# Kernel optimization log

Hardware: AMD Instinct MI355X
Metric: run time of the kernel (lower is better)

The kernel has to match this reference:

```python
import jax, jax.numpy as jnp
import numpy as np

B, K, N, D, H, DD, NB, SEQ = 1, 512, 16384, 512, 64, 64, 10, 2048
COREF_PROP = 1  # config['coref_prop']
BIG = 1e23      # additive mask penalty from the torch code


def bucket_distance(d):
    # Lee et al. style log buckets: 0,1,2,3,4, [5-7], [8-15], [16-31], [32-63], [64+]
    d = jnp.abs(d)
    logb = jnp.floor(jnp.log2(jnp.maximum(d, 1).astype(jnp.float32))).astype(d.dtype) + 3
    return jnp.clip(jnp.where(d < 5, d, logb), 0, NB - 1)


def setup_inputs() -> dict:
    key = jax.random.key(0)
    ks = jax.random.split(key, 20)
    rng = np.random.default_rng(0)
    s = 0.02
    span_begin = jnp.sort(jax.random.randint(ks[2], (B, K), 0, SEQ), axis=-1)
    return dict(
        all_span_vecs=jax.random.normal(ks[0], (B, N, D), jnp.float32),
        span_vecs=jax.random.normal(ks[1], (B, K, D), jnp.float32),
        span_begin=span_begin,
        span_end=span_begin + jax.random.randint(ks[3], (B, K), 1, 10),
        triangular_mask=jnp.broadcast_to(jnp.tril(jnp.ones((K, K), jnp.float32), -1), (B, K, K)),
        span_scores=jax.random.normal(ks[4], (B, K, 1), jnp.float32),
        prune_indices=jnp.asarray(np.sort(np.stack([rng.choice(N, K, replace=False) for _ in range(B)]), axis=-1), jnp.int32),
        span_lengths=jnp.full((B,), K, jnp.int32),
        sequence_lengths=jnp.full((B,), SEQ, jnp.int32),
        Wl=jax.random.normal(ks[5], (D, H)) * s, bl=jnp.zeros((H,), jnp.float32),
        Wr=jax.random.normal(ks[6], (D, H)) * s, br=jnp.zeros((H,), jnp.float32),
        Wp=jax.random.normal(ks[7], (D, H)) * s,
        dist_emb=jax.random.normal(ks[8], (NB, DD)) * s,
        Wd=jax.random.normal(ks[9], (DD, H)) * s, bd=jnp.zeros((H,), jnp.float32),
        Wo=jax.random.normal(ks[10], (H, 1)) * s, bo=jnp.zeros((1,), jnp.float32),
        Wg1=jax.random.normal(ks[11], (2 * D, D)) * s, bg1=jnp.zeros((D,), jnp.float32),
        Wg2=jax.random.normal(ks[12], (2 * D, D)) * s, bg2=jnp.zeros((D,), jnp.float32),
        Wpr=jax.random.normal(ks[13], (D, 1)) * s, bpr=jnp.zeros((1,), jnp.float32),
    )


def reference(all_span_vecs, span_vecs, span_begin, span_end, triangular_mask,
              span_scores, prune_indices, span_lengths, sequence_lengths,
              Wl, bl, Wr, br, Wp, dist_emb, Wd, bd, Wo, bo,
              Wg1, bg1, Wg2, bg2, Wpr, bpr):
    # ----- OptFFpairs pairwise scorer: relu(left_i + right_j + prod(v_i*v_j) + dist_ij) -> scalar
    dist_idx = bucket_distance(span_begin[:, :, None] - span_begin[:, None, :])  # [B,K,K]
    dist_feat = dist_emb[dist_idx] @ Wd + bd                                     # [B,K,K,H]

    def pair_scores(u):
        left = u @ Wl + bl                                  # [B,K,H]
        right = u @ Wr + br                                 # [B,K,H]
        prod = jnp.einsum('bid,bjd,dh->bijh', u, u, Wp)     # avoids [B,K,K,D] intermediate
        h = jax.nn.relu(left[:, :, None, :] + right[:, None, :, :] + prod + dist_feat)
        return (h @ Wo + bo)[..., 0]                        # [B,K,K], i.e. squeeze(-1)

    eye = jnp.eye(K, dtype=span_vecs.dtype)[None]

    def add_scores(cs, ss):  # coref_add_scores: add span scores as rows+cols, zero diagonal
        cs = cs + ss + jnp.swapaxes(ss, -1, -2)
        return cs * (1.0 - eye)

    def gate(Wg, bg, left, right):  # MyGate: g = sigmoid(W[l;r]); g*l + (1-g)*r
        g = jax.nn.sigmoid(jnp.concatenate([left, right], -1) @ Wg + bg)
        return g * left + (1.0 - g) * right

    update = span_vecs
    cs = add_scores(pair_scores(update), span_scores)
    m1 = (1.0 - triangular_mask) * BIG
    m2 = (1.0 - jnp.swapaxes(triangular_mask, 1, 2)) * BIG
    for _ in range(COREF_PROP):
        p1 = jax.nn.softmax(cs - m1, axis=-1)
        p2 = jax.nn.softmax(cs - m2, axis=-1)
        c1 = p1 @ update
        c2 = p2 @ update
        update = gate(Wg1, bg1, update, c1) + gate(Wg2, bg2, update, c2)
        # update_coref_scores=True: rescore with pruner(update)
        cs = add_scores(pair_scores(update), update @ Wpr + bpr)

    # ----- overwrite_spans: masked scatter of updated filtered spans into all spans
    mask = (jnp.arange(K)[None, :] < span_lengths[:, None])[..., None]  # [B,K,1]
    b_idx = jnp.arange(B)[:, None]
    orig = all_span_vecs[b_idx, prune_indices]                          # [B,K,D]
    all_out = all_span_vecs.at[b_idx, prune_indices].set(jnp.where(mask, update, orig))
    return all_out, update, cs
```

## Files before the change

kernel.cpp:

```cpp
#include <hip/hip_runtime.h>
#include <hip/hip_bf16.h>


typedef __bf16 bf16;
typedef bf16 bf16x8 __attribute__((ext_vector_type(8)));
typedef float f32x4 __attribute__((ext_vector_type(4)));
typedef float f32x16 __attribute__((ext_vector_type(16)));

#define MFMA16(a, b, c) __builtin_amdgcn_mfma_f32_16x16x32_bf16((a), (b), (c), 0, 0, 0)
#define MFMA32(a, b, c) __builtin_amdgcn_mfma_f32_32x32x16_bf16((a), (b), (c), 0, 0, 0)

__device__ __forceinline__ void gll16(const bf16* g, bf16* lds) {
  __builtin_amdgcn_global_load_lds(
      (const __attribute__((address_space(1))) unsigned int*)g,
      (__attribute__((address_space(3))) unsigned int*)lds, 16, 0, 0);
}

__global__ void k_prep(const float* __restrict__ sv,
                       const float* __restrict__ Wl, const float* __restrict__ Wr,
                       const float* __restrict__ Wg1, const float* __restrict__ Wg2,
                       const float* __restrict__ de, const float* __restrict__ Wd,
                       const float* __restrict__ bd, const float* __restrict__ bl,
                       const float* __restrict__ br, const float* __restrict__ bg1,
                       const float* __restrict__ bg2, const float* __restrict__ Wp,
                       bf16* __restrict__ u1, bf16* __restrict__ ugb,
                       bf16* __restrict__ wlr, float* __restrict__ blbr,
                       float* __restrict__ bgc, bf16* __restrict__ wgb,
                       float* __restrict__ dtab, bf16* __restrict__ wpTb)
{
  const int total = 262144 + 65536 + 128 + 1048576 + 1024 + 640 + 32768;
  for (int idx0 = blockIdx.x * 256 + threadIdx.x; idx0 < total; idx0 += 2048 * 256) {
    int k = idx0;
    if (k < 262144) {
      float v = sv[k]; bf16 b = (bf16)v; u1[k] = b;
      int i = k >> 9, d = k & 511;
      ugb[(long)i * 1024 + d] = b;
      ugb[524288 + (long)i * 1024 + d] = b;
      continue;
    }
    k -= 262144;
    if (k < 65536) {
      int d = k >> 7, h = k & 127;
      wlr[k] = (bf16)(h < 64 ? Wl[d * 64 + h] : Wr[d * 64 + h - 64]);
      continue;
    }
    k -= 65536;
    if (k < 128) { blbr[k] = (k < 64 ? bl[k] : br[k - 64]); continue; }
    k -= 128;
    if (k < 1048576) {
      wgb[k] = (bf16)(k < 524288 ? Wg1[k] : Wg2[k - 524288]);
      continue;
    }
    k -= 1048576;
    if (k < 1024) { bgc[k] = (k < 512 ? bg1[k] : bg2[k - 512]); continue; }
    k -= 1024;
    if (k < 640) {
      int b_ = k >> 6, h = k & 63;
      float s = bd[h];
      for (int e = 0; e < 64; ++e) s += de[b_ * 64 + e] * Wd[e * 64 + h];
      dtab[k] = s;
      continue;
    }
    k -= 640;
    {
      int h = k >> 9, d = k & 511;
      wpTb[k] = (bf16)Wp[d * 64 + h];
    }
  }
}

__global__ __launch_bounds__(256, 2) void k_gemm(
    const bf16* __restrict__ A, int lda, long asz,
    const bf16* __restrict__ B, int ldb, long bsz,
    float* __restrict__ C, int ldc, long csz,
    const float* __restrict__ bias, int bstride, int K,
    bf16* __restrict__ xout)
{
  __shared__ bf16 As[64 * 40];
  __shared__ bf16 Bs[64 * 40];
  const int t = threadIdx.x, lane = t & 63, wave = t >> 6;
  const int tc = blockIdx.x, tr = blockIdx.y, z = blockIdx.z;
  A += (long)z * asz; B += (long)z * bsz; C += (long)z * csz;
  const int wr = wave >> 1, wc = wave & 1;
  const int arow = t >> 2, aslot = t & 3;
  const int s = lane >> 4, rr = lane & 15;
  f32x4 acc00 = {}, acc01 = {}, acc10 = {}, acc11 = {};
  const int nk = K >> 5;
  for (int kk = 0; kk < nk; ++kk) {
    __syncthreads();
    *(uint4*)&As[arow * 40 + aslot * 8] =
        *(const uint4*)(A + (long)(tr * 64 + arow) * lda + kk * 32 + aslot * 8);
    {
      const bf16* bsrc = B + (long)(kk * 32 + aslot * 8) * ldb + tc * 64 + arow;
      bf16x8 tv;
#pragma unroll
      for (int e = 0; e < 8; ++e) tv[e] = bsrc[(long)e * ldb];
      *(bf16x8*)&Bs[arow * 40 + aslot * 8] = tv;
    }
    __syncthreads();
    bf16x8 a0 = *(const bf16x8*)&As[(wr * 32 + rr) * 40 + s * 8];
    bf16x8 a1 = *(const bf16x8*)&As[(wr * 32 + 16 + rr) * 40 + s * 8];
    bf16x8 b0 = *(const bf16x8*)&Bs[(wc * 32 + rr) * 40 + s * 8];
    bf16x8 b1 = *(const bf16x8*)&Bs[(wc * 32 + 16 + rr) * 40 + s * 8];
    acc00 = MFMA16(a0, b0, acc00);
    acc01 = MFMA16(a0, b1, acc01);
    acc10 = MFMA16(a1, b0, acc10);
    acc11 = MFMA16(a1, b1, acc11);
  }
#pragma unroll
  for (int mf = 0; mf < 2; ++mf) {
#pragma unroll
    for (int nf = 0; nf < 2; ++nf) {
      f32x4 v = mf == 0 ? (nf == 0 ? acc00 : acc01) : (nf == 0 ? acc10 : acc11);
      int col = tc * 64 + wc * 32 + nf * 16 + rr;
      float bi = bias ? bias[z * bstride + col] : 0.f;
      int row0 = tr * 64 + wr * 32 + mf * 16 + s * 4;
#pragma unroll
      for (int r = 0; r < 4; ++r) {
        float val = v[r] + bi;
        int row = row0 + r;
        C[(long)row * ldc + col] = val;
        if (xout) {
          long gidx = (row < 512)
              ? ((long)row * 1024 + 512 + col)
              : (524288 + (long)(row - 512) * 1024 + 512 + col);
          xout[gidx] = (bf16)val;
        }
      }
    }
  }
}

__global__ __launch_bounds__(512, 2) void k_pair(
    const bf16* __restrict__ Ubf, const float* __restrict__ Uf,
    const bf16* __restrict__ wpTb, const float* __restrict__ LR,
    const float* __restrict__ dtabg, const int* __restrict__ sb,
    const float* __restrict__ ss, const float* __restrict__ Wo,
    const float* __restrict__ bo, float* __restrict__ cs,
    const float* __restrict__ copysrc, float* __restrict__ copydst, int docopy)
{
  __shared__ bf16 As[2][512 * 32];
  __shared__ bf16 Vs[2][64 * 32];
  __shared__ float uil[512];
  __shared__ float dts[640];

  const int t = threadIdx.x;
  const int l = t & 63;
  const int w = t >> 6;
  const int i = blockIdx.x;
  const int half = l >> 5;
  const int l31 = l & 31;

  if (t < 128) {
    float4 v = *(const float4*)(Uf + (long)i * 512 + t * 4);
    *(float4*)&uil[t * 4] = v;
  }
  for (int idx = t; idx < 640; idx += 512) dts[idx] = dtabg[idx];

  const bf16 *asrc0, *asrc1, *asrc2, *asrc3;
  {
    int rq0 = 0 * 128 + (t >> 2), rq1 = 1 * 128 + (t >> 2);
    int rq2 = 2 * 128 + (t >> 2), rq3 = 3 * 128 + (t >> 2);
    asrc0 = Ubf + (long)rq0 * 512 + (((t & 3) ^ ((rq0 >> 1) & 3)) * 8);
    asrc1 = Ubf + (long)rq1 * 512 + (((t & 3) ^ ((rq1 >> 1) & 3)) * 8);
    asrc2 = Ubf + (long)rq2 * 512 + (((t & 3) ^ ((rq2 >> 1) & 3)) * 8);
    asrc3 = Ubf + (long)rq3 * 512 + (((t & 3) ^ ((rq3 >> 1) & 3)) * 8);
  }
  int aoff[2][2], voff[2][2];
#pragma unroll
  for (int jf = 0; jf < 2; ++jf)
#pragma unroll
    for (int ks = 0; ks < 2; ++ks) {
      int r = w * 64 + jf * 32 + l31;
      aoff[jf][ks] = r * 64 + (((ks * 2 + half) ^ ((r >> 1) & 3)) * 16);
    }
#pragma unroll
  for (int hf = 0; hf < 2; ++hf)
#pragma unroll
    for (int ks = 0; ks < 2; ++ks) {
      int h = hf * 32 + l31;
      voff[hf][ks] = h * 64 + (((ks * 2 + half) ^ ((h >> 1) & 3)) * 16);
    }
  const int vh = t >> 2;
  const int vcp = (t & 3) ^ ((vh >> 1) & 3);

  __syncthreads();

  gll16(asrc0, &As[0][0 * 4096 + w * 512]);
  gll16(asrc1, &As[0][1 * 4096 + w * 512]);
  gll16(asrc2, &As[0][2 * 4096 + w * 512]);
  gll16(asrc3, &As[0][3 * 4096 + w * 512]);
  if (t < 256) {
    bf16x8 wv = *(const bf16x8*)(wpTb + (long)vh * 512 + vcp * 8);
    float4 u0 = *(const float4*)&uil[vcp * 8];
    float4 u1 = *(const float4*)&uil[vcp * 8 + 4];
    bf16x8 sv8;
#pragma unroll
    for (int e = 0; e < 4; ++e) {
      sv8[e] = (bf16)((float)wv[e] * u0[e]);
      sv8[e + 4] = (bf16)((float)wv[e + 4] * u1[e]);
    }
    *(bf16x8*)((char*)&Vs[0][0] + vh * 64 + (t & 3) * 16) = sv8;
  }
  asm volatile("s_waitcnt vmcnt(0)");
  __syncthreads();

  f32x16 acc[2][2] = {};

  for (int kc = 0; kc < 16; ++kc) {
    const int cur = kc & 1;
    if (kc < 15) {
      gll16(asrc0 + (kc + 1) * 32, &As[cur ^ 1][0 * 4096 + w * 512]);
      gll16(asrc1 + (kc + 1) * 32, &As[cur ^ 1][1 * 4096 + w * 512]);
      gll16(asrc2 + (kc + 1) * 32, &As[cur ^ 1][2 * 4096 + w * 512]);
      gll16(asrc3 + (kc + 1) * 32, &As[cur ^ 1][3 * 4096 + w * 512]);
      if (t < 256) {
        bf16x8 wv = *(const bf16x8*)(wpTb + (long)vh * 512 + (kc + 1) * 32 + vcp * 8);
        float4 u0 = *(const float4*)&uil[(kc + 1) * 32 + vcp * 8];
        float4 u1 = *(const float4*)&uil[(kc + 1) * 32 + vcp * 8 + 4];
        bf16x8 sv8;
#pragma unroll
        for (int e = 0; e < 4; ++e) {
          sv8[e] = (bf16)((float)wv[e] * u0[e]);
          sv8[e + 4] = (bf16)((float)wv[e + 4] * u1[e]);
        }
        *(bf16x8*)((char*)&Vs[cur ^ 1][0] + vh * 64 + (t & 3) * 16) = sv8;
      }
    }
    const char* Asb = (const char*)&As[cur][0];
    const char* Vsb = (const char*)&Vs[cur][0];
#pragma unroll
    for (int ks = 0; ks < 2; ++ks) {
      bf16x8 af0 = *(const bf16x8*)(Asb + aoff[0][ks]);
      bf16x8 af1 = *(const bf16x8*)(Asb + aoff[1][ks]);
      bf16x8 vf0 = *(const bf16x8*)(Vsb + voff[0][ks]);
      bf16x8 vf1 = *(const bf16x8*)(Vsb + voff[1][ks]);
      __builtin_amdgcn_s_setprio(1);
      acc[0][0] = MFMA32(af0, vf0, acc[0][0]);
      acc[0][1] = MFMA32(af0, vf1, acc[0][1]);
      acc[1][0] = MFMA32(af1, vf0, acc[1][0]);
      acc[1][1] = MFMA32(af1, vf1, acc[1][1]);
      __builtin_amdgcn_s_setprio(0);
    }
    if (kc < 15) asm volatile("s_waitcnt vmcnt(0)");
    __syncthreads();
  }

  const float lf0 = LR[i * 128 + l31];
  const float lf1 = LR[i * 128 + 32 + l31];
  const float wo0 = Wo[l31], wo1 = Wo[32 + l31];
  const int sbi = sb[i];
  const float ssi = ss[i];
  const float bo0 = bo[0];
#pragma unroll
  for (int jf = 0; jf < 2; ++jf) {
#pragma unroll
    for (int r = 0; r < 16; ++r) {
      int j = w * 64 + jf * 32 + (r & 3) + 8 * (r >> 2) + 4 * half;
      int dd = sbi - sb[j];
      int ad = dd < 0 ? -dd : dd;
      int bkt = ad < 5 ? ad : (31 - __clz(ad)) + 3;
      bkt = bkt > 9 ? 9 : bkt;
      float v0 = fmaxf(acc[jf][0][r] + lf0 + LR[j * 128 + 64 + l31] +
                       dts[bkt * 64 + l31], 0.f);
      float v1 = fmaxf(acc[jf][1][r] + lf1 + LR[j * 128 + 96 + l31] +
                       dts[bkt * 64 + 32 + l31], 0.f);
      float sum = v0 * wo0 + v1 * wo1;
      sum += __shfl_xor(sum, 1);
      sum += __shfl_xor(sum, 2);
      sum += __shfl_xor(sum, 4);
      sum += __shfl_xor(sum, 8);
      sum += __shfl_xor(sum, 16);
      if (l31 == 0)
        cs[(long)i * 512 + j] = (j == i) ? 0.f : (sum + bo0 + ssi + ss[j]);
    }
  }

  if (docopy) {
    const float4* s4 = (const float4*)copysrc;
    float4* d4 = (float4*)copydst;
    int idx = i * 512 + t;
#pragma unroll
    for (int q = 0; q < 8; ++q)
      d4[(long)q * 262144 + idx] = s4[(long)q * 262144 + idx];
  }
}

__global__ __launch_bounds__(64) void k_softmax(const float* __restrict__ cs,
                                                bf16* __restrict__ p12)
{
  int b = blockIdx.x, kind = b >> 9, i = b & 511, lane = threadIdx.x;
  const float* row = cs + i * 512;
  float v[8];
  float4 x0 = *(const float4*)(row + lane * 8);
  float4 x1 = *(const float4*)(row + lane * 8 + 4);
  v[0] = x0.x; v[1] = x0.y; v[2] = x0.z; v[3] = x0.w;
  v[4] = x1.x; v[5] = x1.y; v[6] = x1.z; v[7] = x1.w;
  bool any = (kind == 0) ? (i > 0) : (i < 511);
  bf16x8 ov;
  if (!any) {
    float u = 1.0f / 512.0f;
#pragma unroll
    for (int e = 0; e < 8; ++e) ov[e] = (bf16)u;
  } else {
    float m = -3.4e38f;
#pragma unroll
    for (int e = 0; e < 8; ++e) {
      int jj = lane * 8 + e;
      bool valid = (kind == 0) ? (jj < i) : (jj > i);
      if (valid) m = fmaxf(m, v[e]);
    }
    m = fmaxf(m, __shfl_xor(m, 1));  m = fmaxf(m, __shfl_xor(m, 2));
    m = fmaxf(m, __shfl_xor(m, 4));  m = fmaxf(m, __shfl_xor(m, 8));
    m = fmaxf(m, __shfl_xor(m, 16)); m = fmaxf(m, __shfl_xor(m, 32));
    float p[8]; float ssum = 0.f;
#pragma unroll
    for (int e = 0; e < 8; ++e) {
      int jj = lane * 8 + e;
      bool valid = (kind == 0) ? (jj < i) : (jj > i);
      p[e] = valid ? __expf(v[e] - m) : 0.f;
      ssum += p[e];
    }
    ssum += __shfl_xor(ssum, 1);  ssum += __shfl_xor(ssum, 2);
    ssum += __shfl_xor(ssum, 4);  ssum += __shfl_xor(ssum, 8);
    ssum += __shfl_xor(ssum, 16); ssum += __shfl_xor(ssum, 32);
    float inv = 1.0f / ssum;
#pragma unroll
    for (int e = 0; e < 8; ++e) ov[e] = (bf16)(p[e] * inv);
  }
  *(bf16x8*)(p12 + (long)b * 512 + lane * 8) = ov;
}

__global__ __launch_bounds__(512) void k_mid2(
    const float* __restrict__ sv, const float* __restrict__ c12,
    const float* __restrict__ G12, const float* __restrict__ Wpr,
    const float* __restrict__ bpr, const bf16* __restrict__ wlr,
    const float* __restrict__ blbr, const int* __restrict__ pi,
    const int* __restrict__ sl, float* __restrict__ upd,
    bf16* __restrict__ u2, float* __restrict__ ss2,
    float* __restrict__ lr2, float* __restrict__ out_all)
{
  __shared__ float upl[512];
  __shared__ float red[8];
  __shared__ float part2[4][128];
  const int i = blockIdx.x;
  const int t = threadIdx.x;
  const long ii = (long)i * 512 + t;

  float u = sv[ii], c1 = c12[ii], c2 = c12[262144 + ii];
  float g1 = 1.f / (1.f + __expf(-G12[ii]));
  float g2 = 1.f / (1.f + __expf(-G12[262144 + ii]));
  float up = g1 * u + (1.f - g1) * c1 + g2 * u + (1.f - g2) * c2;
  upd[ii] = up;
  u2[ii] = (bf16)up;
  upl[t] = up;
  if (i < sl[0]) out_all[(long)pi[i] * 512 + t] = up;

  float pd = up * Wpr[t];
  pd += __shfl_xor(pd, 1);  pd += __shfl_xor(pd, 2);  pd += __shfl_xor(pd, 4);
  pd += __shfl_xor(pd, 8);  pd += __shfl_xor(pd, 16); pd += __shfl_xor(pd, 32);
  if ((t & 63) == 0) red[t >> 6] = pd;
  __syncthreads();
  if (t == 0) {
    float s = 0.f;
#pragma unroll
    for (int e = 0; e < 8; ++e) s += red[e];
    ss2[i] = s + bpr[0];
  }

  const int n = t & 127, part = t >> 7;
  float s = 0.f;
  const int d0 = part * 128;
#pragma unroll 4
  for (int d2 = 0; d2 < 128; ++d2)
    s += upl[d0 + d2] * (float)wlr[(d0 + d2) * 128 + n];
  part2[part][n] = s;
  __syncthreads();
  if (t < 128)
    lr2[(long)i * 128 + t] =
        part2[0][t] + part2[1][t] + part2[2][t] + part2[3][t] + blbr[t];
}

extern "C" void kernel_launch(void* const* d_in, const int* in_sizes, int n_in,
                              void* d_out, int out_size, void* d_ws, size_t ws_size,
                              hipStream_t stream)
{
  const float* asv = (const float*)d_in[0];
  const float* sv = (const float*)d_in[1];
  const int* sb = (const int*)d_in[2];
  const float* sscore = (const float*)d_in[5];
  const int* pi = (const int*)d_in[6];
  const int* sl = (const int*)d_in[7];
  const float* Wl = (const float*)d_in[9];
  const float* bl = (const float*)d_in[10];
  const float* Wr = (const float*)d_in[11];
  const float* br = (const float*)d_in[12];
  const float* Wp = (const float*)d_in[13];
  const float* de = (const float*)d_in[14];
  const float* Wd = (const float*)d_in[15];
  const float* bd = (const float*)d_in[16];
  const float* Wo = (const float*)d_in[17];
  const float* bo = (const float*)d_in[18];
  const float* Wg1 = (const float*)d_in[19];
  const float* bg1 = (const float*)d_in[20];
  const float* Wg2 = (const float*)d_in[21];
  const float* bg2 = (const float*)d_in[22];
  const float* Wpr = (const float*)d_in[23];
  const float* bpr = (const float*)d_in[24];

  float* out_all = (float*)d_out;
  float* out_upd = out_all + 8388608;
  float* out_cs = out_all + 8650752;

  char* w = (char*)d_ws;
  size_t off = 0;
  auto take = [&](size_t bytes) -> void* {
    void* p = w + off;
    off = (off + bytes + 255) & ~(size_t)255;
    return p;
  };
  bf16* u1b = (bf16*)take(524288);
  bf16* u2b = (bf16*)take(524288);
  bf16* wlr = (bf16*)take(131072);
  bf16* wgb = (bf16*)take(2097152);
  float* blbr = (float*)take(512);
  float* bgc = (float*)take(4096);
  float* dtab = (float*)take(2560);
  bf16* wpTb = (bf16*)take(65536);
  float* lr1 = (float*)take(262144);
  float* lr2 = (float*)take(262144);
  float* cs1 = (float*)take(1048576);
  bf16* p12 = (bf16*)take(1048576);
  float* c12 = (float*)take(4194304);
  bf16* ugb = (bf16*)take(2097152);
  float* G12 = (float*)take(2097152);
  float* ss2 = (float*)take(2048);

  k_prep<<<2048, 256, 0, stream>>>(sv, Wl, Wr, Wg1, Wg2, de, Wd, bd, bl, br, bg1, bg2,
                                   Wp, u1b, ugb, wlr, blbr, bgc, wgb, dtab, wpTb);
  k_gemm<<<dim3(2, 8, 1), 256, 0, stream>>>(u1b, 512, 0, wlr, 128, 0, lr1, 128, 0,
                                            blbr, 0, 512, nullptr);
  k_pair<<<512, 512, 0, stream>>>(u1b, sv, wpTb, lr1, dtab, sb, sscore, Wo, bo, cs1,
                                  asv, out_all, 1);
  k_softmax<<<1024, 64, 0, stream>>>(cs1, p12);
  k_gemm<<<dim3(8, 16, 1), 256, 0, stream>>>(p12, 512, 0, u1b, 512, 0, c12, 512, 0,
                                             nullptr, 0, 512, ugb);
  k_gemm<<<dim3(8, 8, 2), 256, 0, stream>>>(ugb, 1024, 524288, wgb, 512, 524288,
                                            G12, 512, 262144, bgc, 512, 1024, nullptr);
  k_mid2<<<512, 512, 0, stream>>>(sv, c12, G12, Wpr, bpr, wlr, blbr, pi, sl,
                                  out_upd, u2b, ss2, lr2, out_all);
  k_pair<<<512, 512, 0, stream>>>(u2b, out_upd, wpTb, lr2, dtab, sb, ss2, Wo, bo,
                                  out_cs, nullptr, nullptr, 0);
}
```

Before: 170.5 us.

## Fold right projection into pair GEMM and reduce Wo via MFMA

The k_pair kernel now adds Wr to the per-row scaled Wp weights, so the right-span projection term is computed inside the main MFMA GEMM instead of gathered per j from LR. The right bias is folded into the left term. The Wo reduction over the hidden dimension is moved from a five-step cross-lane shuffle to staging the ReLU outputs as bf16 in LDS and running a small MFMA against a Wo column. This removes scattered LR loads and shuffles in the epilogue, at the cost of extra bf16 rounding of the hidden activations, an extra weight load per k-chunk, and LDS write/read plus waitcnt barriers.

```diff
diff --git a/kernel.cpp b/kernel.cpp
--- a/kernel.cpp
+++ b/kernel.cpp
@@ -26,9 +26,10 @@
                        bf16* __restrict__ u1, bf16* __restrict__ ugb,
                        bf16* __restrict__ wlr, float* __restrict__ blbr,
                        float* __restrict__ bgc, bf16* __restrict__ wgb,
-                       float* __restrict__ dtab, bf16* __restrict__ wpTb)
-{
-  const int total = 262144 + 65536 + 128 + 1048576 + 1024 + 640 + 32768;
+                       float* __restrict__ dtab, bf16* __restrict__ wpTb,
+                       bf16* __restrict__ wrTb)
+{
+  const int total = 262144 + 65536 + 128 + 1048576 + 1024 + 640 + 32768 + 32768;
   for (int idx0 = blockIdx.x * 256 + threadIdx.x; idx0 < total; idx0 += 2048 * 256) {
     int k = idx0;
     if (k < 262144) {
@@ -62,9 +63,15 @@
       continue;
     }
     k -= 640;
+    if (k < 32768) {
+      int h = k >> 9, d = k & 511;
+      wpTb[k] = (bf16)Wp[d * 64 + h];
+      continue;
+    }
+    k -= 32768;
     {
       int h = k >> 9, d = k & 511;
-      wpTb[k] = (bf16)Wp[d * 64 + h];
+      wrTb[k] = (bf16)Wr[d * 64 + h];
     }
   }
 }
@@ -133,10 +140,11 @@
 
 __global__ __launch_bounds__(512, 2) void k_pair(
     const bf16* __restrict__ Ubf, const float* __restrict__ Uf,
-    const bf16* __restrict__ wpTb, const float* __restrict__ LR,
-    const float* __restrict__ dtabg, const int* __restrict__ sb,
-    const float* __restrict__ ss, const float* __restrict__ Wo,
-    const float* __restrict__ bo, float* __restrict__ cs,
+    const bf16* __restrict__ wpTb, const bf16* __restrict__ wrTb,
+    const float* __restrict__ LR, const float* __restrict__ dtabg,
+    const int* __restrict__ sb, const float* __restrict__ ss,
+    const float* __restrict__ Wo, const float* __restrict__ bo,
+    const float* __restrict__ Br, float* __restrict__ cs,
     const float* __restrict__ copysrc, float* __restrict__ copydst, int docopy)
 {
   __shared__ bf16 As[2][512 * 32];
@@ -192,13 +200,14 @@
   gll16(asrc3, &As[0][3 * 4096 + w * 512]);
   if (t < 256) {
     bf16x8 wv = *(const bf16x8*)(wpTb + (long)vh * 512 + vcp * 8);
+    bf16x8 wr8 = *(const bf16x8*)(wrTb + (long)vh * 512 + vcp * 8);
     float4 u0 = *(const float4*)&uil[vcp * 8];
     float4 u1 = *(const float4*)&uil[vcp * 8 + 4];
     bf16x8 sv8;
 #pragma unroll
     for (int e = 0; e < 4; ++e) {
-      sv8[e] = (bf16)((float)wv[e] * u0[e]);
-      sv8[e + 4] = (bf16)((float)wv[e + 4] * u1[e]);
+      sv8[e] = (bf16)((float)wv[e] * u0[e] + (float)wr8[e]);
+      sv8[e + 4] = (bf16)((float)wv[e + 4] * u1[e] + (float)wr8[e + 4]);
     }
     *(bf16x8*)((char*)&Vs[0][0] + vh * 64 + (t & 3) * 16) = sv8;
   }
@@ -216,13 +225,14 @@
       gll16(asrc3 + (kc + 1) * 32, &As[cur ^ 1][3 * 4096 + w * 512]);
       if (t < 256) {
         bf16x8 wv = *(const bf16x8*)(wpTb + (long)vh * 512 + (kc + 1) * 32 + vcp * 8);
+        bf16x8 wr8 = *(const bf16x8*)(wrTb + (long)vh * 512 + (kc + 1) * 32 + vcp * 8);
         float4 u0 = *(const float4*)&uil[(kc + 1) * 32 + vcp * 8];
         float4 u1 = *(const float4*)&uil[(kc + 1) * 32 + vcp * 8 + 4];
         bf16x8 sv8;
 #pragma unroll
         for (int e = 0; e < 4; ++e) {
-          sv8[e] = (bf16)((float)wv[e] * u0[e]);
-          sv8[e + 4] = (bf16)((float)wv[e + 4] * u1[e]);
+          sv8[e] = (bf16)((float)wv[e] * u0[e] + (float)wr8[e]);
+          sv8[e + 4] = (bf16)((float)wv[e + 4] * u1[e] + (float)wr8[e + 4]);
         }
         *(bf16x8*)((char*)&Vs[cur ^ 1][0] + vh * 64 + (t & 3) * 16) = sv8;
       }
@@ -246,34 +256,55 @@
     __syncthreads();
   }
 
-  const float lf0 = LR[i * 128 + l31];
-  const float lf1 = LR[i * 128 + 32 + l31];
-  const float wo0 = Wo[l31], wo1 = Wo[32 + l31];
+  const float lf0 = LR[i * 128 + l31] + Br[l31];
+  const float lf1 = LR[i * 128 + 32 + l31] + Br[32 + l31];
+  bf16x8 wob[4];
+#pragma unroll
+  for (int c = 0; c < 4; ++c) {
+#pragma unroll
+    for (int e = 0; e < 8; ++e)
+      wob[c][e] = (l31 == 0) ? (bf16)Wo[c * 16 + half * 8 + e] : (bf16)0.f;
+  }
   const int sbi = sb[i];
   const float ssi = ss[i];
   const float bo0 = bo[0];
+  char* T = (char*)&As[0][0] + w * 4096;
+
 #pragma unroll
   for (int jf = 0; jf < 2; ++jf) {
 #pragma unroll
     for (int r = 0; r < 16; ++r) {
-      int j = w * 64 + jf * 32 + (r & 3) + 8 * (r >> 2) + 4 * half;
+      int jl = (r & 3) + 8 * (r >> 2) + 4 * half;
+      int j = w * 64 + jf * 32 + jl;
       int dd = sbi - sb[j];
       int ad = dd < 0 ? -dd : dd;
       int bkt = ad < 5 ? ad : (31 - __clz(ad)) + 3;
       bkt = bkt > 9 ? 9 : bkt;
-      float v0 = fmaxf(acc[jf][0][r] + lf0 + LR[j * 128 + 64 + l31] +
-                       dts[bkt * 64 + l31], 0.f);
-      float v1 = fmaxf(acc[jf][1][r] + lf1 + LR[j * 128 + 96 + l31] +
-                       dts[bkt * 64 + 32 + l31], 0.f);
-      float sum = v0 * wo0 + v1 * wo1;
-      sum += __shfl_xor(sum, 1);
-      sum += __shfl_xor(sum, 2);
-      sum += __shfl_xor(sum, 4);
-      sum += __shfl_xor(sum, 8);
-      sum += __shfl_xor(sum, 16);
-      if (l31 == 0)
-        cs[(long)i * 512 + j] = (j == i) ? 0.f : (sum + bo0 + ssi + ss[j]);
-    }
+      float v0 = fmaxf(acc[jf][0][r] + lf0 + dts[bkt * 64 + l31], 0.f);
+      float v1 = fmaxf(acc[jf][1][r] + lf1 + dts[bkt * 64 + 32 + l31], 0.f);
+      char* rowp = T + jl * 128;
+      *(bf16*)(rowp + (((l31 >> 3) ^ (jl & 7)) * 16) + (l31 & 7) * 2) = (bf16)v0;
+      *(bf16*)(rowp + ((((l31 >> 3) + 4) ^ (jl & 7)) * 16) + (l31 & 7) * 2) = (bf16)v1;
+    }
+    asm volatile("s_waitcnt lgkmcnt(0)" ::: "memory");
+    __builtin_amdgcn_sched_barrier(0);
+    f32x16 acc2 = {};
+#pragma unroll
+    for (int c = 0; c < 4; ++c) {
+      bf16x8 afr = *(const bf16x8*)(T + l31 * 128 + (((c * 2 + half) ^ (l31 & 7)) * 16));
+      acc2 = MFMA32(afr, wob[c], acc2);
+    }
+    if (l31 == 0) {
+#pragma unroll
+      for (int r = 0; r < 16; ++r) {
+        int jl = (r & 3) + 8 * (r >> 2) + 4 * half;
+        int j = w * 64 + jf * 32 + jl;
+        float val = acc2[r] + bo0 + ssi + ss[j];
+        cs[(long)i * 512 + j] = (j == i) ? 0.f : val;
+      }
+    }
+    asm volatile("s_waitcnt lgkmcnt(0)" ::: "memory");
+    __builtin_amdgcn_sched_barrier(0);
   }
 
   if (docopy) {
@@ -427,6 +458,7 @@
   float* bgc = (float*)take(4096);
   float* dtab = (float*)take(2560);
   bf16* wpTb = (bf16*)take(65536);
+  bf16* wrTb = (bf16*)take(65536);
   float* lr1 = (float*)take(262144);
   float* lr2 = (float*)take(262144);
   float* cs1 = (float*)take(1048576);
@@ -437,11 +469,11 @@
   float* ss2 = (float*)take(2048);
 
   k_prep<<<2048, 256, 0, stream>>>(sv, Wl, Wr, Wg1, Wg2, de, Wd, bd, bl, br, bg1, bg2,
-                                   Wp, u1b, ugb, wlr, blbr, bgc, wgb, dtab, wpTb);
+                                   Wp, u1b, ugb, wlr, blbr, bgc, wgb, dtab, wpTb, wrTb);
   k_gemm<<<dim3(2, 8, 1), 256, 0, stream>>>(u1b, 512, 0, wlr, 128, 0, lr1, 128, 0,
                                             blbr, 0, 512, nullptr);
-  k_pair<<<512, 512, 0, stream>>>(u1b, sv, wpTb, lr1, dtab, sb, sscore, Wo, bo, cs1,
-                                  asv, out_all, 1);
+  k_pair<<<512, 512, 0, stream>>>(u1b, sv, wpTb, wrTb, lr1, dtab, sb, sscore, Wo, bo,
+                                  br, cs1, asv, out_all, 1);
   k_softmax<<<1024, 64, 0, stream>>>(cs1, p12);
   k_gemm<<<dim3(8, 16, 1), 256, 0, stream>>>(p12, 512, 0, u1b, 512, 0, c12, 512, 0,
                                              nullptr, 0, 512, ugb);
@@ -449,6 +481,6 @@
                                             G12, 512, 262144, bgc, 512, 1024, nullptr);
   k_mid2<<<512, 512, 0, stream>>>(sv, c12, G12, Wpr, bpr, wlr, blbr, pi, sl,
                                   out_upd, u2b, ss2, lr2, out_all);
-  k_pair<<<512, 512, 0, stream>>>(u2b, out_upd, wpTb, lr2, dtab, sb, ss2, Wo, bo,
-                                  out_cs, nullptr, nullptr, 0);
-}
+  k_pair<<<512, 512, 0, stream>>>(u2b, out_upd, wpTb, wrTb, lr2, dtab, sb, ss2, Wo, bo,
+                                  br, out_cs, nullptr, nullptr, 0);
+}
```

Result: slower. 186.3 us (+9.2%).

## Retile pair-score kernel to 4 rows × 256 cols per block with shared B panel

Applied to the files above, without the earlier changes.

The pair-score kernel used to process one mention row per block and reload the full 512×512 bf16 span matrix for every row. It now gives each block 4 query rows and a 256-column tile. The scaled A panel (u_i * Wp) is built in registers, and the B panel of span vectors is shared across the 4 rows. This cuts global and LDS traffic for the B operand about 4x and gives each wave more MFMAs per fragment load. The epilogue reduction also changes to per-lane accumulation over the hidden dimension with a single cross-half shuffle. In exchange it uses more accumulator registers, and the A-panel products are built from global loads inside the k-loop.

```diff
diff --git a/kernel.cpp b/kernel.cpp
--- a/kernel.cpp
+++ b/kernel.cpp
@@ -139,150 +139,176 @@
     const float* __restrict__ bo, float* __restrict__ cs,
     const float* __restrict__ copysrc, float* __restrict__ copydst, int docopy)
 {
-  __shared__ bf16 As[2][512 * 32];
-  __shared__ bf16 Vs[2][64 * 32];
-  __shared__ float uil[512];
-  __shared__ float dts[640];
+  __shared__ bf16 Apan[2][256 * 32];
+  __shared__ bf16 Bpan[2][256 * 32];
+  __shared__ float dtsp[10 * 68];
+  __shared__ int sbt[256];
 
   const int t = threadIdx.x;
   const int l = t & 63;
   const int w = t >> 6;
-  const int i = blockIdx.x;
-  const int half = l >> 5;
-  const int l31 = l & 31;
-
-  if (t < 128) {
-    float4 v = *(const float4*)(Uf + (long)i * 512 + t * 4);
-    *(float4*)&uil[t * 4] = v;
-  }
-  for (int idx = t; idx < 640; idx += 512) dts[idx] = dtabg[idx];
-
-  const bf16 *asrc0, *asrc1, *asrc2, *asrc3;
+  const int wm = w >> 1, wn = w & 1;
+  const int hi = l >> 5, l31 = l & 31;
+  const int jb = blockIdx.x;
+  const int mt = blockIdx.y;
+  const int i0 = mt * 4;
+  const int i = i0 + wm;
+
+  for (int idx = t; idx < 640; idx += 512)
+    dtsp[(idx >> 6) * 68 + (idx & 63)] = dtabg[idx];
+  if (t < 256) sbt[t] = sb[jb * 256 + t];
+
+  const bf16 *bsrc0, *bsrc1;
   {
-    int rq0 = 0 * 128 + (t >> 2), rq1 = 1 * 128 + (t >> 2);
-    int rq2 = 2 * 128 + (t >> 2), rq3 = 3 * 128 + (t >> 2);
-    asrc0 = Ubf + (long)rq0 * 512 + (((t & 3) ^ ((rq0 >> 1) & 3)) * 8);
-    asrc1 = Ubf + (long)rq1 * 512 + (((t & 3) ^ ((rq1 >> 1) & 3)) * 8);
-    asrc2 = Ubf + (long)rq2 * 512 + (((t & 3) ^ ((rq2 >> 1) & 3)) * 8);
-    asrc3 = Ubf + (long)rq3 * 512 + (((t & 3) ^ ((rq3 >> 1) & 3)) * 8);
-  }
-  int aoff[2][2], voff[2][2];
-#pragma unroll
-  for (int jf = 0; jf < 2; ++jf)
+    int r0 = t >> 2, c0 = t & 3;
+    int r1 = 128 + (t >> 2);
+    bsrc0 = Ubf + (long)(jb * 256 + r0) * 512 + ((c0 ^ ((r0 >> 1) & 3)) * 8);
+    bsrc1 = Ubf + (long)(jb * 256 + r1) * 512 + ((c0 ^ ((r1 >> 1) & 3)) * 8);
+  }
+  const int ar0 = t >> 2, ar1 = 128 + (t >> 2), as0 = t & 3;
+  const int awb0 = ar0 * 64 + ((as0 ^ ((ar0 >> 1) & 3)) * 16);
+  const int awb1 = ar1 * 64 + ((as0 ^ ((ar1 >> 1) & 3)) * 16);
+  const float* ua0p = Uf + (long)(i0 + (ar0 >> 6)) * 512 + as0 * 8;
+  const float* ua1p = Uf + (long)(i0 + (ar1 >> 6)) * 512 + as0 * 8;
+  const bf16* wp0p = wpTb + (long)(ar0 & 63) * 512 + as0 * 8;
+  const bf16* wp1p = wpTb + (long)(ar1 & 63) * 512 + as0 * 8;
+
+  int aoff[2][2], boff[4][2];
+#pragma unroll
+  for (int rf = 0; rf < 2; ++rf)
 #pragma unroll
     for (int ks = 0; ks < 2; ++ks) {
-      int r = w * 64 + jf * 32 + l31;
-      aoff[jf][ks] = r * 64 + (((ks * 2 + half) ^ ((r >> 1) & 3)) * 16);
-    }
-#pragma unroll
-  for (int hf = 0; hf < 2; ++hf)
+      int r = wm * 64 + rf * 32 + l31;
+      aoff[rf][ks] = r * 64 + (((ks * 2 + hi) ^ ((r >> 1) & 3)) * 16);
+    }
+#pragma unroll
+  for (int cf = 0; cf < 4; ++cf)
 #pragma unroll
     for (int ks = 0; ks < 2; ++ks) {
-      int h = hf * 32 + l31;
-      voff[hf][ks] = h * 64 + (((ks * 2 + half) ^ ((h >> 1) & 3)) * 16);
-    }
-  const int vh = t >> 2;
-  const int vcp = (t & 3) ^ ((vh >> 1) & 3);
-
-  __syncthreads();
-
-  gll16(asrc0, &As[0][0 * 4096 + w * 512]);
-  gll16(asrc1, &As[0][1 * 4096 + w * 512]);
-  gll16(asrc2, &As[0][2 * 4096 + w * 512]);
-  gll16(asrc3, &As[0][3 * 4096 + w * 512]);
-  if (t < 256) {
-    bf16x8 wv = *(const bf16x8*)(wpTb + (long)vh * 512 + vcp * 8);
-    float4 u0 = *(const float4*)&uil[vcp * 8];
-    float4 u1 = *(const float4*)&uil[vcp * 8 + 4];
-    bf16x8 sv8;
+      int r = wn * 128 + cf * 32 + l31;
+      boff[cf][ks] = r * 64 + (((ks * 2 + hi) ^ ((r >> 1) & 3)) * 16);
+    }
+
+  {
+    gll16(bsrc0, &Bpan[0][0 * 4096 + w * 512]);
+    gll16(bsrc1, &Bpan[0][1 * 4096 + w * 512]);
+    float4 a00 = *(const float4*)ua0p, a01 = *(const float4*)(ua0p + 4);
+    float4 a10 = *(const float4*)ua1p, a11 = *(const float4*)(ua1p + 4);
+    bf16x8 w0 = *(const bf16x8*)wp0p, w1 = *(const bf16x8*)wp1p;
+    bf16x8 v0, v1;
 #pragma unroll
     for (int e = 0; e < 4; ++e) {
-      sv8[e] = (bf16)((float)wv[e] * u0[e]);
-      sv8[e + 4] = (bf16)((float)wv[e + 4] * u1[e]);
-    }
-    *(bf16x8*)((char*)&Vs[0][0] + vh * 64 + (t & 3) * 16) = sv8;
+      v0[e] = (bf16)(a00[e] * (float)w0[e]);
+      v0[e + 4] = (bf16)(a01[e] * (float)w0[e + 4]);
+      v1[e] = (bf16)(a10[e] * (float)w1[e]);
+      v1[e + 4] = (bf16)(a11[e] * (float)w1[e + 4]);
+    }
+    *(bf16x8*)((char*)&Apan[0][0] + awb0) = v0;
+    *(bf16x8*)((char*)&Apan[0][0] + awb1) = v1;
   }
   asm volatile("s_waitcnt vmcnt(0)");
   __syncthreads();
 
-  f32x16 acc[2][2] = {};
+  f32x16 acc[2][4] = {};
 
   for (int kc = 0; kc < 16; ++kc) {
     const int cur = kc & 1;
+    float4 nA00, nA01, nA10, nA11;
+    bf16x8 nW0, nW1;
     if (kc < 15) {
-      gll16(asrc0 + (kc + 1) * 32, &As[cur ^ 1][0 * 4096 + w * 512]);
-      gll16(asrc1 + (kc + 1) * 32, &As[cur ^ 1][1 * 4096 + w * 512]);
-      gll16(asrc2 + (kc + 1) * 32, &As[cur ^ 1][2 * 4096 + w * 512]);
-      gll16(asrc3 + (kc + 1) * 32, &As[cur ^ 1][3 * 4096 + w * 512]);
-      if (t < 256) {
-        bf16x8 wv = *(const bf16x8*)(wpTb + (long)vh * 512 + (kc + 1) * 32 + vcp * 8);
-        float4 u0 = *(const float4*)&uil[(kc + 1) * 32 + vcp * 8];
-        float4 u1 = *(const float4*)&uil[(kc + 1) * 32 + vcp * 8 + 4];
-        bf16x8 sv8;
+      gll16(bsrc0 + (kc + 1) * 32, &Bpan[cur ^ 1][0 * 4096 + w * 512]);
+      gll16(bsrc1 + (kc + 1) * 32, &Bpan[cur ^ 1][1 * 4096 + w * 512]);
+      nA00 = *(const float4*)(ua0p + (kc + 1) * 32);
+      nA01 = *(const float4*)(ua0p + (kc + 1) * 32 + 4);
+      nA10 = *(const float4*)(ua1p + (kc + 1) * 32);
+      nA11 = *(const float4*)(ua1p + (kc + 1) * 32 + 4);
+      nW0 = *(const bf16x8*)(wp0p + (kc + 1) * 32);
+      nW1 = *(const bf16x8*)(wp1p + (kc + 1) * 32);
+    }
+    const char* Ab = (const char*)&Apan[cur][0];
+    const char* Bb = (const char*)&Bpan[cur][0];
+#pragma unroll
+    for (int ks = 0; ks < 2; ++ks) {
+      bf16x8 af0 = *(const bf16x8*)(Ab + aoff[0][ks]);
+      bf16x8 af1 = *(const bf16x8*)(Ab + aoff[1][ks]);
+      bf16x8 bf0 = *(const bf16x8*)(Bb + boff[0][ks]);
+      bf16x8 bf1 = *(const bf16x8*)(Bb + boff[1][ks]);
+      bf16x8 bf2 = *(const bf16x8*)(Bb + boff[2][ks]);
+      bf16x8 bf3 = *(const bf16x8*)(Bb + boff[3][ks]);
+      __builtin_amdgcn_s_setprio(1);
+      acc[0][0] = MFMA32(af0, bf0, acc[0][0]);
+      acc[0][1] = MFMA32(af0, bf1, acc[0][1]);
+      acc[0][2] = MFMA32(af0, bf2, acc[0][2]);
+      acc[0][3] = MFMA32(af0, bf3, acc[0][3]);
+      acc[1][0] = MFMA32(af1, bf0, acc[1][0]);
+      acc[1][1] = MFMA32(af1, bf1, acc[1][1]);
+      acc[1][2] = MFMA32(af1, bf2, acc[1][2]);
+      acc[1][3] = MFMA32(af1, bf3, acc[1][3]);
+      __builtin_amdgcn_s_setprio(0);
+    }
+    if (kc < 15) {
+      asm volatile("s_waitcnt vmcnt(0)");
+      bf16x8 v0, v1;
+#pragma unroll
+      for (int e = 0; e < 4; ++e) {
+        v0[e] = (bf16)(nA00[e] * (float)nW0[e]);
+        v0[e + 4] = (bf16)(nA01[e] * (float)nW0[e + 4]);
+        v1[e] = (bf16)(nA10[e] * (float)nW1[e]);
+        v1[e + 4] = (bf16)(nA11[e] * (float)nW1[e + 4]);
+      }
+      *(bf16x8*)((char*)&Apan[cur ^ 1][0] + awb0) = v0;
+      *(bf16x8*)((char*)&Apan[cur ^ 1][0] + awb1) = v1;
+    }
+    __syncthreads();
+  }
+
+  float4 wo_t[2][4], lf_t[2][4];
+#pragma unroll
+  for (int rf = 0; rf < 2; ++rf)
+#pragma unroll
+    for (int g = 0; g < 4; ++g) {
+      wo_t[rf][g] = *(const float4*)&Wo[rf * 32 + 4 * hi + 8 * g];
+      lf_t[rf][g] = *(const float4*)&LR[i * 128 + rf * 32 + 4 * hi + 8 * g];
+    }
+  const float ssi = ss[i];
+  const int sbi = sb[i];
+  const float bo0 = bo[0];
+#pragma unroll
+  for (int cf = 0; cf < 4; ++cf) {
+    int jl = wn * 128 + cf * 32 + l31;
+    int j = jb * 256 + jl;
+    int dd = sbi - sbt[jl];
+    int ad = dd < 0 ? -dd : dd;
+    int bkt = ad < 5 ? ad : (31 - __clz(ad)) + 3;
+    bkt = bkt > 9 ? 9 : bkt;
+    float ssj = ss[j];
+    float sum = 0.f;
+#pragma unroll
+    for (int rf = 0; rf < 2; ++rf) {
+#pragma unroll
+      for (int g = 0; g < 4; ++g) {
+        float4 dt4 = *(const float4*)&dtsp[bkt * 68 + rf * 32 + 4 * hi + 8 * g];
+        float4 rt4 = *(const float4*)&LR[j * 128 + 64 + rf * 32 + 4 * hi + 8 * g];
 #pragma unroll
         for (int e = 0; e < 4; ++e) {
-          sv8[e] = (bf16)((float)wv[e] * u0[e]);
-          sv8[e + 4] = (bf16)((float)wv[e + 4] * u1[e]);
+          float v = acc[rf][cf][g * 4 + e] + lf_t[rf][g][e] + rt4[e] + dt4[e];
+          v = fmaxf(v, 0.f);
+          sum += v * wo_t[rf][g][e];
         }
-        *(bf16x8*)((char*)&Vs[cur ^ 1][0] + vh * 64 + (t & 3) * 16) = sv8;
       }
     }
-    const char* Asb = (const char*)&As[cur][0];
-    const char* Vsb = (const char*)&Vs[cur][0];
-#pragma unroll
-    for (int ks = 0; ks < 2; ++ks) {
-      bf16x8 af0 = *(const bf16x8*)(Asb + aoff[0][ks]);
-      bf16x8 af1 = *(const bf16x8*)(Asb + aoff[1][ks]);
-      bf16x8 vf0 = *(const bf16x8*)(Vsb + voff[0][ks]);
-      bf16x8 vf1 = *(const bf16x8*)(Vsb + voff[1][ks]);
-      __builtin_amdgcn_s_setprio(1);
-      acc[0][0] = MFMA32(af0, vf0, acc[0][0]);
-      acc[0][1] = MFMA32(af0, vf1, acc[0][1]);
-      acc[1][0] = MFMA32(af1, vf0, acc[1][0]);
-      acc[1][1] = MFMA32(af1, vf1, acc[1][1]);
-      __builtin_amdgcn_s_setprio(0);
-    }
-    if (kc < 15) asm volatile("s_waitcnt vmcnt(0)");
-    __syncthreads();
-  }
-
-  const float lf0 = LR[i * 128 + l31];
-  const float lf1 = LR[i * 128 + 32 + l31];
-  const float wo0 = Wo[l31], wo1 = Wo[32 + l31];
-  const int sbi = sb[i];
-  const float ssi = ss[i];
-  const float bo0 = bo[0];
-#pragma unroll
-  for (int jf = 0; jf < 2; ++jf) {
-#pragma unroll
-    for (int r = 0; r < 16; ++r) {
-      int j = w * 64 + jf * 32 + (r & 3) + 8 * (r >> 2) + 4 * half;
-      int dd = sbi - sb[j];
-      int ad = dd < 0 ? -dd : dd;
-      int bkt = ad < 5 ? ad : (31 - __clz(ad)) + 3;
-      bkt = bkt > 9 ? 9 : bkt;
-      float v0 = fmaxf(acc[jf][0][r] + lf0 + LR[j * 128 + 64 + l31] +
-                       dts[bkt * 64 + l31], 0.f);
-      float v1 = fmaxf(acc[jf][1][r] + lf1 + LR[j * 128 + 96 + l31] +
-                       dts[bkt * 64 + 32 + l31], 0.f);
-      float sum = v0 * wo0 + v1 * wo1;
-      sum += __shfl_xor(sum, 1);
-      sum += __shfl_xor(sum, 2);
-      sum += __shfl_xor(sum, 4);
-      sum += __shfl_xor(sum, 8);
-      sum += __shfl_xor(sum, 16);
-      if (l31 == 0)
-        cs[(long)i * 512 + j] = (j == i) ? 0.f : (sum + bo0 + ssi + ss[j]);
-    }
+    sum += __shfl_xor(sum, 32);
+    float val = (j == i) ? 0.f : (sum + bo0 + ssi + ssj);
+    if (hi == 0) cs[(long)i * 512 + j] = val;
   }
 
   if (docopy) {
     const float4* s4 = (const float4*)copysrc;
     float4* d4 = (float4*)copydst;
-    int idx = i * 512 + t;
-#pragma unroll
-    for (int q = 0; q < 8; ++q)
-      d4[(long)q * 262144 + idx] = s4[(long)q * 262144 + idx];
+    int idx = (mt * 2 + jb) * 512 + t;
+#pragma unroll
+    for (int q = 0; q < 16; ++q)
+      d4[(long)q * 131072 + idx] = s4[(long)q * 131072 + idx];
   }
 }
 
@@ -440,8 +466,8 @@
                                    Wp, u1b, ugb, wlr, blbr, bgc, wgb, dtab, wpTb);
   k_gemm<<<dim3(2, 8, 1), 256, 0, stream>>>(u1b, 512, 0, wlr, 128, 0, lr1, 128, 0,
                                             blbr, 0, 512, nullptr);
-  k_pair<<<512, 512, 0, stream>>>(u1b, sv, wpTb, lr1, dtab, sb, sscore, Wo, bo, cs1,
-                                  asv, out_all, 1);
+  k_pair<<<dim3(2, 128), 512, 0, stream>>>(u1b, sv, wpTb, lr1, dtab, sb, sscore, Wo,
+                                           bo, cs1, asv, out_all, 1);
   k_softmax<<<1024, 64, 0, stream>>>(cs1, p12);
   k_gemm<<<dim3(8, 16, 1), 256, 0, stream>>>(p12, 512, 0, u1b, 512, 0, c12, 512, 0,
                                              nullptr, 0, 512, ugb);
@@ -449,6 +475,6 @@
                                             G12, 512, 262144, bgc, 512, 1024, nullptr);
   k_mid2<<<512, 512, 0, stream>>>(sv, c12, G12, Wpr, bpr, wlr, blbr, pi, sl,
                                   out_upd, u2b, ss2, lr2, out_all);
-  k_pair<<<512, 512, 0, stream>>>(u2b, out_upd, wpTb, lr2, dtab, sb, ss2, Wo, bo,
-                                  out_cs, nullptr, nullptr, 0);
-}
+  k_pair<<<dim3(2, 128), 512, 0, stream>>>(u2b, out_upd, wpTb, lr2, dtab, sb, ss2, Wo,
+                                           bo, out_cs, nullptr, nullptr, 0);
+}
```

Measured after the change: 148.1 us. 13.2% less time.
